# Optimization experiments

Hardware: AMD Instinct MI355X
Metric: run time of the kernel (lower is better)

The kernel has to match this reference:

```python
import jax, jax.numpy as jnp
import numpy as np

EPS = 1e-5

def conv2d(x, w, b, pad):
    y = jax.lax.conv_general_dilated(x, w, (1, 1), [(pad, pad), (pad, pad)],
                                     dimension_numbers=('NCHW', 'OIHW', 'NCHW'))
    return y + b[None, :, None, None]

def batchnorm(x, g, be):
    # training-mode BN: biased batch statistics over (N,H,W)
    m = x.mean(axis=(0, 2, 3), keepdims=True)
    v = x.var(axis=(0, 2, 3), keepdims=True)
    return (x - m) * jax.lax.rsqrt(v + EPS) * g[None, :, None, None] + be[None, :, None, None]

def _bilinear_gather(x_flat, ys, xs, H, W):
    # x_flat: [B,C,H*W]; ys,xs: [B,H,W] float sample coords; zero outside borders
    y0f = jnp.floor(ys); x0f = jnp.floor(xs)
    wy = (ys - y0f)[:, None]; wx = (xs - x0f)[:, None]   # [B,1,H,W]
    y0 = y0f.astype(jnp.int32); x0 = x0f.astype(jnp.int32)

    def corner(iy, ix):
        valid = ((iy >= 0) & (iy < H) & (ix >= 0) & (ix < W)).astype(x_flat.dtype)
        idx = jnp.clip(iy, 0, H - 1) * W + jnp.clip(ix, 0, W - 1)   # [B,H,W]
        v = jax.vmap(lambda xf, i: xf[:, i])(x_flat, idx)           # [B,C,H,W]
        return v * valid[:, None]

    v00 = corner(y0, x0);     v01 = corner(y0, x0 + 1)
    v10 = corner(y0 + 1, x0); v11 = corner(y0 + 1, x0 + 1)
    return v00 * (1 - wy) * (1 - wx) + v01 * (1 - wy) * wx + v10 * wy * (1 - wx) + v11 * wy * wx

def dcn(x, w, b, ow, ob):
    # modulated deformable conv (DCNv2), k=3, stride=1, pad=1
    B, C, H, W = x.shape
    K = 9
    om = conv2d(x, ow, ob, 1)                 # [B,27,H,W]
    dy = om[:, :K]; dx = om[:, K:2 * K]; m = jax.nn.sigmoid(om[:, 2 * K:])
    x_flat = x.reshape(B, C, H * W)
    base_y = jnp.arange(H, dtype=x.dtype)[None, :, None]
    base_x = jnp.arange(W, dtype=x.dtype)[None, None, :]
    out = jnp.zeros((B, w.shape[0], H, W), dtype=x.dtype)
    for k in range(K):  # fixed 9 kernel taps
        ky, kx = k // 3 - 1, k % 3 - 1
        ys = base_y + ky + dy[:, k]
        xs = base_x + kx + dx[:, k]
        samp = _bilinear_gather(x_flat, ys, xs, H, W)        # [B,C,H,W]
        out = out + jnp.einsum('bchw,oc->bohw', samp * m[:, k][:, None], w[:, :, k // 3, k % 3])
    return out + b[None, :, None, None]

def setup_inputs() -> dict:
    key = jax.random.key(0)
    ks = iter(jax.random.split(key, 64))
    B, H, W, C = 2, 256, 256, 64
    NB = 16
    f32 = jnp.float32
    d = {}
    for name in ['LowDEM', 'Point_Ele', 'Slope', 'Distance', 'Level']:
        d[name] = jax.random.normal(next(ks), (B, 1, H, W), dtype=f32)
    s = 0.05
    d['conv0_w'] = jax.random.normal(next(ks), (1, 3, 1, 1), f32) * s
    d['conv0_b'] = jnp.zeros((1,), f32)
    d['conv1_w'] = jax.random.normal(next(ks), (C, 1, 9, 9), f32) * s
    d['conv1_b'] = jnp.zeros((C,), f32)
    d['rb_w1'] = jax.random.normal(next(ks), (NB, C, C, 3, 3), f32) * s
    d['rb_b1'] = jnp.zeros((NB, C), f32)
    d['rb_g1'] = jnp.ones((NB, C), f32)
    d['rb_be1'] = jnp.zeros((NB, C), f32)
    d['rb_w2'] = jax.random.normal(next(ks), (NB, C, C, 3, 3), f32) * s
    d['rb_b2'] = jnp.zeros((NB, C), f32)
    d['rb_g2'] = jnp.ones((NB, C), f32)
    d['rb_be2'] = jnp.zeros((NB, C), f32)
    d['conv2_w'] = jax.random.normal(next(ks), (C, C, 3, 3), f32) * s
    d['conv2_b'] = jnp.zeros((C,), f32)
    d['bn2_g'] = jnp.ones((C,), f32)
    d['bn2_be'] = jnp.zeros((C,), f32)
    for nm, cout in [('dc2', C), ('dc3', C), ('dc4', 1)]:
        d[nm + '_w'] = jax.random.normal(next(ks), (cout, C, 3, 3), f32) * s
        d[nm + '_b'] = jnp.zeros((cout,), f32)
        d[nm + '_ow'] = jax.random.normal(next(ks), (27, C, 3, 3), f32) * 0.01
        d[nm + '_ob'] = jnp.zeros((27,), f32)
    d['conv4_w'] = jax.random.normal(next(ks), (1, 1, 1, 1), f32) * s
    d['conv4_b'] = jnp.zeros((1,), f32)
    return d

def reference(LowDEM, Point_Ele, Slope, Distance, Level,
              conv0_w, conv0_b, conv1_w, conv1_b,
              rb_w1, rb_b1, rb_g1, rb_be1, rb_w2, rb_b2, rb_g2, rb_be2,
              conv2_w, conv2_b, bn2_g, bn2_be,
              dc2_w, dc2_b, dc2_ow, dc2_ob,
              dc3_w, dc3_b, dc3_ow, dc3_ob,
              dc4_w, dc4_b, dc4_ow, dc4_ob,
              conv4_w, conv4_b):
    data = jnp.concatenate([Slope, Distance, Level], axis=1)
    error = conv2d(data, conv0_w, conv0_b, 0)
    lmask = (Level != 0).astype(LowDEM.dtype)
    error = error * lmask
    x = LowDEM * (1.0 - lmask) + Point_Ele + error
    x = conv2d(x, conv1_w, conv1_b, 4)
    y = x
    for i in range(rb_w1.shape[0]):  # fixed 16 residual blocks
        r = jax.nn.relu(batchnorm(conv2d(y, rb_w1[i], rb_b1[i], 1), rb_g1[i], rb_be1[i]))
        y = batchnorm(conv2d(r, rb_w2[i], rb_b2[i], 1), rb_g2[i], rb_be2[i]) + y
    x = batchnorm(conv2d(y, conv2_w, conv2_b, 1), bn2_g, bn2_be) + x
    x = jax.nn.relu(dcn(x, dc2_w, dc2_b, dc2_ow, dc2_ob))
    x = jax.nn.relu(dcn(x, dc3_w, dc3_b, dc3_ow, dc3_ob))
    x = dcn(x, dc4_w, dc4_b, dc4_ow, dc4_ob)
    return conv2d(x, conv4_w, conv4_b, 0)
```

## Files before the change

kernel.cpp:

```cpp
#include <hip/hip_runtime.h>
#include <cmath>

typedef unsigned short ushort_t;
typedef __attribute__((ext_vector_type(8))) short bf16x8;
typedef __attribute__((ext_vector_type(4))) float f32x4;

static constexpr int Bn   = 2;
static constexpr int Hn   = 256;
static constexpr int Wn   = 256;
static constexpr int HW   = Hn * Wn;
static constexpr int CHW  = 64 * HW;
static constexpr int NCHW = Bn * CHW;
static constexpr int NPIX = Bn * HW;
static constexpr float EPSv = 1e-5f;
static constexpr float INV_N = 1.0f / 131072.0f;
static constexpr int NSLOT = 64;
static constexpr int STSLOT = NSLOT * 128;
static constexpr int WFL = 73728;

__device__ inline uint32_t bf16_rne(float f) {
  uint32_t u = __float_as_uint(f);
  return (u + 0x7FFFu + ((u >> 16) & 1u)) >> 16;
}
__device__ inline void split_hl(float v, uint32_t& h, uint32_t& l) {
  h = bf16_rne(v);
  l = bf16_rne(v - __uint_as_float(h << 16)) & 0xFFFFu;
}
__device__ inline bf16x8 lds_ld16(const ushort_t* p) {
  union { bf16x8 v; uint2 u[2]; } r;
  r.u[0] = *(const uint2*)p;
  r.u[1] = *(const uint2*)(p + 4);
  return r.v;
}

typedef __attribute__((address_space(1))) const void glb_void;
typedef __attribute__((address_space(3))) void lds_void;
__device__ inline void gld_lds16(const void* g, void* l) {
  __builtin_amdgcn_global_load_lds((glb_void*)g, (lds_void*)l, 16, 0, 0);
}

__global__ void transpose_w_kernel(const float* __restrict__ in, float* __restrict__ out,
                                   int NB, int OC, int IC, int K) {
  int total = NB * OC * IC * K;
  for (int i = blockIdx.x * blockDim.x + threadIdx.x; i < total; i += gridDim.x * blockDim.x) {
    int k  = i % K;
    int t  = i / K;
    int ic = t % IC; t /= IC;
    int oc = t % OC;
    int nb = t / OC;
    out[(((size_t)nb * IC + ic) * K + k) * OC + oc] = in[i];
  }
}

__global__ void prep_wfrag(const float* __restrict__ w, ushort_t* __restrict__ out,
                           int NGp, int ocreal, int wlstride, int olstride) {
  int layer = blockIdx.y;
  int elems = 9 * 2 * NGp * 64 * 8;
  int idx = blockIdx.x * 256 + threadIdx.x;
  if (idx >= elems) return;
  int j = idx & 7, lane = (idx >> 3) & 63;
  int rest = idx >> 9;
  int g = rest % NGp; rest /= NGp;
  int ih = rest & 1, tap = rest >> 1;
  int oc = g * 16 + (lane & 15);
  int ic = ih * 32 + (lane >> 4) * 8 + j;
  float v = 0.0f;
  if (oc < ocreal) v = w[(size_t)layer * wlstride + (oc * 64 + ic) * 9 + tap];
  uint32_t hi, lo;
  split_hl(v, hi, lo);
  out[(size_t)layer * olstride + idx] = (ushort_t)hi;
  out[(size_t)layer * olstride + elems + idx] = (ushort_t)lo;
}

__global__ void prep_kernel(const float* __restrict__ LowDEM, const float* __restrict__ Point_Ele,
                            const float* __restrict__ Slope, const float* __restrict__ Distance,
                            const float* __restrict__ Level, const float* __restrict__ w0,
                            const float* __restrict__ b0, float* __restrict__ x0) {
  int i = blockIdx.x * blockDim.x + threadIdx.x;
  if (i >= NPIX) return;
  float lv  = Level[i];
  float err = w0[0] * Slope[i] + w0[1] * Distance[i] + w0[2] * lv + b0[0];
  float lm  = (lv != 0.0f) ? 1.0f : 0.0f;
  x0[i] = LowDEM[i] * (1.0f - lm) + Point_Ele[i] + err * lm;
}

__global__ __launch_bounds__(256, 2)
void conv9x9_kernel(const float* __restrict__ in, const float* __restrict__ wT,
                    const float* __restrict__ bias, float* __restrict__ out,
                    uint32_t* __restrict__ hiP, uint32_t* __restrict__ loP) {
  const int tx = threadIdx.x & 15, ty = threadIdx.x >> 4;
  const int w0 = blockIdx.x * 16, h0 = blockIdx.y * 16, b = blockIdx.z;
  __shared__ float lds[24 * 24];
  for (int idx = threadIdx.x; idx < 576; idx += 256) {
    int yy = idx / 24, xx = idx - yy * 24;
    int gy = h0 + yy - 4, gx = w0 + xx - 4;
    float v = 0.0f;
    if ((unsigned)gy < 256u && (unsigned)gx < 256u) v = in[b * HW + gy * 256 + gx];
    lds[idx] = v;
  }
  __syncthreads();
  float acc[64];
#pragma unroll
  for (int o = 0; o < 64; o++) acc[o] = 0.0f;
#pragma unroll 1
  for (int i = 0; i < 9; i++) {
#pragma unroll
    for (int j = 0; j < 9; j++) {
      float v = lds[(ty + i) * 24 + tx + j];
      const float* wp = wT + (i * 9 + j) * 64;
#pragma unroll
      for (int o = 0; o < 64; o++) acc[o] = fmaf(v, wp[o], acc[o]);
    }
  }
  const int p = (h0 + ty) * 256 + (w0 + tx);
  if (hiP) {
    float* op = out + ((size_t)b * HW + p) * 64;
#pragma unroll
    for (int o4 = 0; o4 < 16; o4++) {
      float4 v;
      v.x = acc[o4 * 4 + 0] + bias[o4 * 4 + 0];
      v.y = acc[o4 * 4 + 1] + bias[o4 * 4 + 1];
      v.z = acc[o4 * 4 + 2] + bias[o4 * 4 + 2];
      v.w = acc[o4 * 4 + 3] + bias[o4 * 4 + 3];
      *(float4*)(op + o4 * 4) = v;
    }
    uint32_t* hb = hiP + ((size_t)b * HW + p) * 32;
    uint32_t* lb = loP + ((size_t)b * HW + p) * 32;
#pragma unroll
    for (int o2 = 0; o2 < 32; o2++) {
      float v0 = acc[o2 * 2] + bias[o2 * 2];
      float v1 = acc[o2 * 2 + 1] + bias[o2 * 2 + 1];
      uint32_t h0v, l0v, h1v, l1v;
      split_hl(v0, h0v, l0v);
      split_hl(v1, h1v, l1v);
      hb[o2] = h0v | (h1v << 16);
      lb[o2] = l0v | (l1v << 16);
    }
  } else {
    float* op = out + (size_t)b * CHW + p;
#pragma unroll
    for (int o = 0; o < 64; o++) op[o * HW] = acc[o] + bias[o];
  }
}

template <int NG, int MODE, int STATS, int OCLIM, int HASBIAS, int WRITEY, int INHWC>
__global__ __launch_bounds__(256, 3)
void mfma_conv3(const float* __restrict__ in, const float* __restrict__ skip,
                const ushort_t* __restrict__ wf,
                const float* __restrict__ bias, const float* __restrict__ stats_in,
                const float* __restrict__ gg, const float* __restrict__ be,
                float* __restrict__ stats_out, float* __restrict__ yout,
                float* __restrict__ out) {
  const int tid  = threadIdx.x;
  const int lane = tid & 63, wid = tid >> 6;
  const int m = lane & 15, quad = lane >> 4;
  const int x0 = blockIdx.x * 16, y0 = blockIdx.y * 4, b = blockIdx.z;
  constexpr int WT = 2 * NG * 64 * 8;
  __shared__ __align__(16) ushort_t xh[108 * 68];
  __shared__ __align__(16) ushort_t xl[108 * 68];
  __shared__ float s_sc[MODE ? 64 : 1], s_sh[MODE ? 64 : 1];
  __shared__ float red[STATS ? 2 * 4 * 64 : 1];
  if (MODE) {
    if (tid < 64) {
      float sum = 0.0f, sq = 0.0f;
      for (int sl = 0; sl < NSLOT; sl++) {
        sum += stats_in[sl * 128 + tid];
        sq  += stats_in[sl * 128 + 64 + tid];
      }
      float mn = sum * INV_N, var = sq * INV_N - mn * mn;
      float s = gg[tid] * rsqrtf(var + EPSv);
      s_sc[tid] = s;
      s_sh[tid] = be[tid] - mn * s;
    }
    __syncthreads();
  }
  const float* inb = in + (size_t)b * CHW;
  const float* skb = MODE == 2 ? skip + (size_t)b * CHW : nullptr;
  float* ytb = WRITEY ? yout + (size_t)b * CHW : nullptr;
  uint32_t* xh32 = (uint32_t*)xh;
  uint32_t* xl32 = (uint32_t*)xl;
#pragma unroll
  for (int t = 0; t < 14; t++) {
    int idx = t * 256 + tid;
    if (idx < 3456) {
      int r, icp;
      if (INHWC) { icp = idx & 31; r = idx >> 5; }
      else       { r = idx % 108; icp = idx / 108; }
      int row = r / 18, col = r - row * 18;
      int gy = y0 - 1 + row, gx = x0 - 1 + col;
      float v0 = 0.0f, v1 = 0.0f;
      if ((unsigned)gy < 256u && (unsigned)gx < 256u) {
        int ic = icp * 2;
        if (INHWC) {
          float2 vv = *(const float2*)&inb[(size_t)(gy * 256 + gx) * 64 + ic];
          v0 = vv.x; v1 = vv.y;
        } else {
          v0 = inb[ic * HW + gy * 256 + gx];
          v1 = inb[(ic + 1) * HW + gy * 256 + gx];
        }
        if (MODE == 1) {
          v0 = fmaxf(fmaf(v0, s_sc[ic], s_sh[ic]), 0.0f);
          v1 = fmaxf(fmaf(v1, s_sc[ic + 1], s_sh[ic + 1]), 0.0f);
        }
        if (MODE == 2) {
          v0 = fmaf(v0, s_sc[ic], s_sh[ic]) + skb[ic * HW + gy * 256 + gx];
          v1 = fmaf(v1, s_sc[ic + 1], s_sh[ic + 1]) + skb[(ic + 1) * HW + gy * 256 + gx];
          if (WRITEY && row >= 1 && row <= 4 && col >= 1 && col <= 16) {
            ytb[ic * HW + gy * 256 + gx] = v0;
            ytb[(ic + 1) * HW + gy * 256 + gx] = v1;
          }
        }
      }
      uint32_t h0, l0, h1, l1;
      split_hl(v0, h0, l0);
      split_hl(v1, h1, l1);
      xh32[r * 34 + icp] = h0 | (h1 << 16);
      xl32[r * 34 + icp] = l0 | (l1 << 16);
    }
  }
  __syncthreads();
  f32x4 acc[NG];
#pragma unroll
  for (int g = 0; g < NG; g++) acc[g] = (f32x4){0.0f, 0.0f, 0.0f, 0.0f};

  const bf16x8* wfh = (const bf16x8*)wf;
  const bf16x8* wfl = (const bf16x8*)(wf + 9 * WT);

#pragma unroll 1
  for (int tap = 0; tap < 9; tap++) {
    bf16x8 bh[2][NG], bl[2][NG];
#pragma unroll
    for (int ih = 0; ih < 2; ih++)
#pragma unroll
      for (int g = 0; g < NG; g++) {
        int fi = ((tap * 2 + ih) * NG + g) * 64 + lane;
        bh[ih][g] = wfh[fi];
        bl[ih][g] = wfl[fi];
      }
    const int dy = tap / 3 - 1, dx = tap % 3 - 1;
    const int spat = (wid + dy + 1) * 18 + (m + dx + 1);
#pragma unroll
    for (int ih = 0; ih < 2; ih++) {
      const int base = spat * 68 + ih * 32 + quad * 8;
      bf16x8 ah = lds_ld16(xh + base);
      bf16x8 al = lds_ld16(xl + base);
#pragma unroll
      for (int g = 0; g < NG; g++) {
        acc[g] = __builtin_amdgcn_mfma_f32_16x16x32_bf16(ah, bh[ih][g], acc[g], 0, 0, 0);
        acc[g] = __builtin_amdgcn_mfma_f32_16x16x32_bf16(al, bh[ih][g], acc[g], 0, 0, 0);
        acc[g] = __builtin_amdgcn_mfma_f32_16x16x32_bf16(ah, bl[ih][g], acc[g], 0, 0, 0);
      }
    }
  }
  const int py = y0 + wid;
  float* ob = out + (size_t)b * OCLIM * HW + py * 256 + x0 + quad * 4;
#pragma unroll
  for (int g = 0; g < NG; g++) {
    int oc = g * 16 + m;
    if (oc < OCLIM) {
      float bv = HASBIAS ? bias[oc] : 0.0f;
#pragma unroll
      for (int r = 0; r < 4; r++) ob[oc * HW + r] = acc[g][r] + bv;
    }
    if (STATS) {
      float s  = acc[g][0] + acc[g][1] + acc[g][2] + acc[g][3];
      float s2 = acc[g][0] * acc[g][0] + acc[g][1] * acc[g][1] +
                 acc[g][2] * acc[g][2] + acc[g][3] * acc[g][3];
      s  += __shfl_xor(s, 16, 64);  s  += __shfl_xor(s, 32, 64);
      s2 += __shfl_xor(s2, 16, 64); s2 += __shfl_xor(s2, 32, 64);
      if (lane < 16) {
        red[(0 * 4 + wid) * 64 + g * 16 + lane] = s;
        red[(1 * 4 + wid) * 64 + g * 16 + lane] = s2;
      }
    }
  }
  if (STATS) {
    __syncthreads();
    if (tid < 128) {
      int oc = tid & 63, which = tid >> 6;
      float tot = red[(which * 4 + 0) * 64 + oc] + red[(which * 4 + 1) * 64 + oc] +
                  red[(which * 4 + 2) * 64 + oc] + red[(which * 4 + 3) * 64 + oc];
      int slot = (blockIdx.y * 16 + blockIdx.x) & (NSLOT - 1);
      atomicAdd(&stats_out[slot * 128 + which * 64 + oc], tot);
    }
  }
}

__global__ __launch_bounds__(256, 3)
void mfma_conv3_dma(const ushort_t* __restrict__ hiP, const ushort_t* __restrict__ loP,
                    const ushort_t* __restrict__ wf, const float* __restrict__ zeroPg,
                    float* __restrict__ stats_out, float* __restrict__ out) {
  const int tid  = threadIdx.x;
  const int lane = tid & 63, wid = tid >> 6;
  const int m = lane & 15, quad = lane >> 4;
  const int x0 = blockIdx.x * 16, y0 = blockIdx.y * 8, b = blockIdx.z;
  __shared__ __align__(16) ushort_t xs[2880 * 8];
  __shared__ float red[2 * 4 * 64];
  const size_t bimg = (size_t)b * HW;
  for (int g = wid; g < 45; g += 4) {
    int q  = g * 64 + lane;
    int pl = q >= 1440;
    int r  = q - (pl ? 1440 : 0);
    int s  = r >> 3, jl = r & 7;
    int js = jl ^ (s & 7);
    int row = s / 18, col = s - row * 18;
    int gy = y0 - 1 + row, gx = x0 - 1 + col;
    const ushort_t* src = (const ushort_t*)zeroPg;
    if ((unsigned)gy < 256u && (unsigned)gx < 256u)
      src = (pl ? loP : hiP) + ((bimg + (size_t)(gy * 256 + gx)) << 6) + (js << 3);
    gld_lds16(src, (void*)&xs[(size_t)g * 512]);
  }
  __syncthreads();

  f32x4 acc[2][4];
#pragma unroll
  for (int t = 0; t < 2; t++)
#pragma unroll
    for (int g = 0; g < 4; g++) acc[t][g] = (f32x4){0.0f, 0.0f, 0.0f, 0.0f};
  const bf16x8* wfh = (const bf16x8*)wf;
  const bf16x8* wfl8 = (const bf16x8*)(wf + 9 * 4096);

#pragma unroll 1
  for (int tap = 0; tap < 9; tap++) {
    bf16x8 bh[2][4], bl[2][4];
#pragma unroll
    for (int ih = 0; ih < 2; ih++)
#pragma unroll
      for (int g = 0; g < 4; g++) {
        int fi = ((tap * 2 + ih) * 4 + g) * 64 + lane;
        bh[ih][g] = wfh[fi];
        bl[ih][g] = wfl8[fi];
      }
    const int dy = tap / 3 - 1, dxx = tap % 3 - 1;
    const int scol = m + dxx + 1;
#pragma unroll
    for (int t = 0; t < 2; t++) {
      const int s  = (wid * 2 + t + dy + 1) * 18 + scol;
      const int s7 = s & 7;
#pragma unroll
      for (int ih = 0; ih < 2; ih++) {
        const int ch = s * 8 + ((ih * 4 + quad) ^ s7);
        bf16x8 ah = *(const bf16x8*)&xs[ch * 8];
        bf16x8 al = *(const bf16x8*)&xs[ch * 8 + 11520];
#pragma unroll
        for (int g = 0; g < 4; g++) {
          acc[t][g] = __builtin_amdgcn_mfma_f32_16x16x32_bf16(ah, bh[ih][g], acc[t][g], 0, 0, 0);
          acc[t][g] = __builtin_amdgcn_mfma_f32_16x16x32_bf16(al, bh[ih][g], acc[t][g], 0, 0, 0);
          acc[t][g] = __builtin_amdgcn_mfma_f32_16x16x32_bf16(ah, bl[ih][g], acc[t][g], 0, 0, 0);
        }
      }
    }
  }
#pragma unroll
  for (int g = 0; g < 4; g++) {
    int oc = g * 16 + m;
    float s = 0.0f, s2 = 0.0f;
#pragma unroll
    for (int t = 0; t < 2; t++) {
      const int py = y0 + wid * 2 + t;
      float* ob = out + ((size_t)b * HW + (size_t)py * 256 + x0) * 64;
#pragma unroll
      for (int r = 0; r < 4; r++) {
        float v = acc[t][g][r];
        ob[(quad * 4 + r) * 64 + oc] = v;
        s += v;
        s2 += v * v;
      }
    }
    s  += __shfl_xor(s, 16, 64);  s  += __shfl_xor(s, 32, 64);
    s2 += __shfl_xor(s2, 16, 64); s2 += __shfl_xor(s2, 32, 64);
    if (lane < 16) {
      red[(0 * 4 + wid) * 64 + g * 16 + lane] = s;
      red[(1 * 4 + wid) * 64 + g * 16 + lane] = s2;
    }
  }
  __syncthreads();
  if (tid < 128) {
    int oc = tid & 63, which = tid >> 6;
    float tot = red[(which * 4 + 0) * 64 + oc] + red[(which * 4 + 1) * 64 + oc] +
                red[(which * 4 + 2) * 64 + oc] + red[(which * 4 + 3) * 64 + oc];
    int slot = (blockIdx.y * 16 + blockIdx.x) & (NSLOT - 1);
    atomicAdd(&stats_out[slot * 128 + which * 64 + oc], tot);
  }
}

__global__ __launch_bounds__(256, 3)
void ofs_conv_dma(const ushort_t* __restrict__ hiP, const ushort_t* __restrict__ loP,
                  const ushort_t* __restrict__ wf, const float* __restrict__ zeroPg,
                  const float* __restrict__ bias, float* __restrict__ out) {
  const int tid  = threadIdx.x;
  const int lane = tid & 63, wid = tid >> 6;
  const int m = lane & 15, quad = lane >> 4;
  const int x0 = blockIdx.x * 16, y0 = blockIdx.y * 8, b = blockIdx.z;
  __shared__ __align__(16) ushort_t xs[2880 * 8];
  const size_t bimg = (size_t)b * HW;
  for (int g = wid; g < 45; g += 4) {
    int q  = g * 64 + lane;
    int pl = q >= 1440;
    int r  = q - (pl ? 1440 : 0);
    int s  = r >> 3, jl = r & 7;
    int js = jl ^ (s & 7);
    int row = s / 18, col = s - row * 18;
    int gy = y0 - 1 + row, gx = x0 - 1 + col;
    const ushort_t* src = (const ushort_t*)zeroPg;
    if ((unsigned)gy < 256u && (unsigned)gx < 256u)
      src = (pl ? loP : hiP) + ((bimg + (size_t)(gy * 256 + gx)) << 6) + (js << 3);
    gld_lds16(src, (void*)&xs[(size_t)g * 512]);
  }
  __syncthreads();

  f32x4 acc[2][2];
#pragma unroll
  for (int t = 0; t < 2; t++)
#pragma unroll
    for (int g = 0; g < 2; g++) acc[t][g] = (f32x4){0.0f, 0.0f, 0.0f, 0.0f};
  const bf16x8* wfh = (const bf16x8*)wf;
  const bf16x8* wfl8 = (const bf16x8*)(wf + 9 * 2048);

#pragma unroll 1
  for (int tap = 0; tap < 9; tap++) {
    bf16x8 bh[2][2], bl[2][2];
#pragma unroll
    for (int ih = 0; ih < 2; ih++)
#pragma unroll
      for (int g = 0; g < 2; g++) {
        int fi = ((tap * 2 + ih) * 2 + g) * 64 + lane;
        bh[ih][g] = wfh[fi];
        bl[ih][g] = wfl8[fi];
      }
    const int dy = tap / 3 - 1, dxx = tap % 3 - 1;
    const int scol = m + dxx + 1;
#pragma unroll
    for (int t = 0; t < 2; t++) {
      const int s  = (wid * 2 + t + dy + 1) * 18 + scol;
      const int s7 = s & 7;
#pragma unroll
      for (int ih = 0; ih < 2; ih++) {
        const int ch = s * 8 + ((ih * 4 + quad) ^ s7);
        bf16x8 ah = *(const bf16x8*)&xs[ch * 8];
        bf16x8 al = *(const bf16x8*)&xs[ch * 8 + 11520];
#pragma unroll
        for (int g = 0; g < 2; g++) {
          acc[t][g] = __builtin_amdgcn_mfma_f32_16x16x32_bf16(ah, bh[ih][g], acc[t][g], 0, 0, 0);
          acc[t][g] = __builtin_amdgcn_mfma_f32_16x16x32_bf16(al, bh[ih][g], acc[t][g], 0, 0, 0);
          acc[t][g] = __builtin_amdgcn_mfma_f32_16x16x32_bf16(ah, bl[ih][g], acc[t][g], 0, 0, 0);
        }
      }
    }
  }
#pragma unroll
  for (int g = 0; g < 2; g++) {
    int oc = g * 16 + m;
    if (oc < 27) {
      float bv = bias[oc];
#pragma unroll
      for (int t = 0; t < 2; t++) {
        const int py = y0 + wid * 2 + t;
        float* ob = out + (size_t)b * 27 * HW + (size_t)oc * HW + py * 256 + x0 + quad * 4;
#pragma unroll
        for (int r = 0; r < 4; r++) ob[r] = acc[t][g][r] + bv;
      }
    }
  }
}

template <int TMODE>
__global__ __launch_bounds__(256, 8)
void bn_split_hwc(const float* __restrict__ t, const float* __restrict__ stats,
                  const float* __restrict__ g, const float* __restrict__ be,
                  const float* __restrict__ skip, float* __restrict__ yout,
                  uint32_t* __restrict__ hiP, uint32_t* __restrict__ loP) {
  __shared__ float part[2][4][64];
  __shared__ float s_sc[64], s_sh[64];
  const int tid = threadIdx.x;
  {
    int c = tid & 63, q = tid >> 6;
    float sum = 0.0f, sq = 0.0f;
    for (int sl = q * 16; sl < q * 16 + 16; sl++) {
      sum += stats[sl * 128 + c];
      sq  += stats[sl * 128 + 64 + c];
    }
    part[0][q][c] = sum;
    part[1][q][c] = sq;
  }
  __syncthreads();
  if (tid < 64) {
    int c = tid;
    float sum = part[0][0][c] + part[0][1][c] + part[0][2][c] + part[0][3][c];
    float sq  = part[1][0][c] + part[1][1][c] + part[1][2][c] + part[1][3][c];
    float mn  = sum * INV_N;
    float var = sq * INV_N - mn * mn;
    float s   = g[c] * rsqrtf(var + EPSv);
    s_sc[c] = s;
    s_sh[c] = be[c] - mn * s;
  }
  __syncthreads();
  const int blk = blockIdx.x;
  const int b  = blk >> 10;
  const int p0 = (blk & 1023) * 64;
  const size_t base = ((size_t)b * HW + p0) * 64;
  uint32_t* hb = hiP + ((size_t)b * HW + p0) * 32;
  uint32_t* lb = loP + ((size_t)b * HW + p0) * 32;
#pragma unroll
  for (int i = 0; i < 8; i++) {
    int idx = i * 256 + tid;
    int p = idx >> 5, c2 = idx & 31;
    size_t off = base + (size_t)p * 64 + c2 * 2;
    float2 v = *(const float2*)&t[off];
    float v0 = fmaf(v.x, s_sc[c2 * 2],     s_sh[c2 * 2]);
    float v1 = fmaf(v.y, s_sc[c2 * 2 + 1], s_sh[c2 * 2 + 1]);
    if (TMODE == 1) {
      v0 = fmaxf(v0, 0.0f);
      v1 = fmaxf(v1, 0.0f);
    } else {
      float2 k = *(const float2*)&skip[off];
      v0 += k.x; v1 += k.y;
      float2 y2; y2.x = v0; y2.y = v1;
      *(float2*)&yout[off] = y2;
    }
    uint32_t h0v, l0v, h1v, l1v;
    split_hl(v0, h0v, l0v);
    split_hl(v1, h1v, l1v);
    hb[p * 32 + c2] = h0v | (h1v << 16);
    lb[p * 32 + c2] = l0v | (l1v << 16);
  }
}

__global__ __launch_bounds__(256, 8)
void bn_add_hwc(const float* __restrict__ t, const float* __restrict__ stats,
                const float* __restrict__ g, const float* __restrict__ be,
                const float* __restrict__ skip, float* __restrict__ xout,
                uint32_t* __restrict__ hiP, uint32_t* __restrict__ loP) {
  __shared__ float part[2][4][64];
  __shared__ float s_sc[64], s_sh[64];
  const int tid = threadIdx.x;
  {
    int c = tid & 63, q = tid >> 6;
    float sum = 0.0f, sq = 0.0f;
    for (int sl = q * 16; sl < q * 16 + 16; sl++) {
      sum += stats[sl * 128 + c];
      sq  += stats[sl * 128 + 64 + c];
    }
    part[0][q][c] = sum;
    part[1][q][c] = sq;
  }
  __syncthreads();
  if (tid < 64) {
    int c = tid;
    float sum = part[0][0][c] + part[0][1][c] + part[0][2][c] + part[0][3][c];
    float sq  = part[1][0][c] + part[1][1][c] + part[1][2][c] + part[1][3][c];
    float mn  = sum * INV_N;
    float var = sq * INV_N - mn * mn;
    float s   = g[c] * rsqrtf(var + EPSv);
    s_sc[c] = s;
    s_sh[c] = be[c] - mn * s;
  }
  __syncthreads();
  const int blk = blockIdx.x;
  const int b  = blk >> 10;
  const int p0 = (blk & 1023) * 64;
  const size_t base4 = (((size_t)b * HW + p0) * 64) >> 2;
  const float4* t4 = (const float4*)t;
  const float4* k4 = (const float4*)skip;
  float4* x4 = (float4*)xout;
  uint32_t* hb = hiP + ((size_t)b * HW + p0) * 32;
  uint32_t* lb = loP + ((size_t)b * HW + p0) * 32;
#pragma unroll
  for (int i = 0; i < 4; i++) {
    int idx = i * 256 + tid;
    int c = (idx & 15) * 4;
    int p = idx >> 4;
    float4 v = t4[base4 + idx], k = k4[base4 + idx], r;
    r.x = fmaf(v.x, s_sc[c],     s_sh[c])     + k.x;
    r.y = fmaf(v.y, s_sc[c + 1], s_sh[c + 1]) + k.y;
    r.z = fmaf(v.z, s_sc[c + 2], s_sh[c + 2]) + k.z;
    r.w = fmaf(v.w, s_sc[c + 3], s_sh[c + 3]) + k.w;
    x4[base4 + idx] = r;
    uint32_t h0v, l0v, h1v, l1v, h2v, l2v, h3v, l3v;
    split_hl(r.x, h0v, l0v); split_hl(r.y, h1v, l1v);
    split_hl(r.z, h2v, l2v); split_hl(r.w, h3v, l3v);
    uint2 hv = make_uint2(h0v | (h1v << 16), h2v | (h3v << 16));
    uint2 lv = make_uint2(l0v | (l1v << 16), l2v | (l3v << 16));
    *(uint2*)&hb[p * 32 + (c >> 1)] = hv;
    *(uint2*)&lb[p * 32 + (c >> 1)] = lv;
  }
}

__global__ void bn_apply_add_kernel(const float* __restrict__ t, const float* __restrict__ stats,
                                    const float* __restrict__ g, const float* __restrict__ be,
                                    const float* __restrict__ skip, float* __restrict__ out) {
  __shared__ float s_sc[64], s_sh[64];
  if (threadIdx.x < 64) {
    int c = threadIdx.x;
    float sum = 0.0f, sq = 0.0f;
    for (int sl = 0; sl < NSLOT; sl++) {
      sum += stats[sl * 128 + c];
      sq  += stats[sl * 128 + 64 + c];
    }
    float m   = sum * INV_N;
    float var = sq * INV_N - m * m;
    float s   = g[c] * rsqrtf(var + EPSv);
    s_sc[c] = s;
    s_sh[c] = be[c] - m * s;
  }
  __syncthreads();
  const float4* t4 = (const float4*)t;
  const float4* k4 = (const float4*)skip;
  float4* o4 = (float4*)out;
  const int n4 = NCHW / 4;
  for (int i = blockIdx.x * blockDim.x + threadIdx.x; i < n4; i += gridDim.x * blockDim.x) {
    int c = (i >> 14) & 63;
    float s = s_sc[c], h = s_sh[c];
    float4 v = t4[i], kk = k4[i], r;
    r.x = fmaf(v.x, s, h) + kk.x;
    r.y = fmaf(v.y, s, h) + kk.y;
    r.z = fmaf(v.z, s, h) + kk.z;
    r.w = fmaf(v.w, s, h) + kk.w;
    o4[i] = r;
  }
}

__global__ __launch_bounds__(256, 4)
void bn_tx_kernel(const float* __restrict__ t, const float* __restrict__ stats,
                  const float* __restrict__ g, const float* __restrict__ be,
                  const float* __restrict__ skip, float* __restrict__ outP,
                  float* __restrict__ outHWC) {
  __shared__ float tile[64][65];
  __shared__ float s_sc[64], s_sh[64];
  if (threadIdx.x < 64) {
    int c = threadIdx.x;
    float sum = 0.0f, sq = 0.0f;
    for (int sl = 0; sl < NSLOT; sl++) {
      sum += stats[sl * 128 + c];
      sq  += stats[sl * 128 + 64 + c];
    }
    float m   = sum * INV_N;
    float var = sq * INV_N - m * m;
    float s   = g[c] * rsqrtf(var + EPSv);
    s_sc[c] = s;
    s_sh[c] = be[c] - m * s;
  }
  __syncthreads();
  const int blk = blockIdx.x;
  const int b = blk >> 10;
  const int p0 = (blk & 1023) * 64;
  const float* tb = t + (size_t)b * CHW;
  const float* kb = skip + (size_t)b * CHW;
  float* oP = outP + (size_t)b * CHW;
  float* oH = outHWC + (size_t)b * CHW;
#pragma unroll
  for (int i = 0; i < 16; i++) {
    int idx = i * 256 + threadIdx.x;
    int c = idx >> 6, p = idx & 63;
    float v = fmaf(tb[c * HW + p0 + p], s_sc[c], s_sh[c]) + kb[c * HW + p0 + p];
    oP[c * HW + p0 + p] = v;
    tile[c][p] = v;
  }
  __syncthreads();
#pragma unroll
  for (int i = 0; i < 16; i++) {
    int idx = i * 256 + threadIdx.x;
    int p = idx >> 6, c = idx & 63;
    oH[(size_t)(p0 + p) * 64 + c] = tile[c][p];
  }
}

template <int NG, int FINAL>
__global__ __launch_bounds__(256, 4)
void dcn_mfma(const float* __restrict__ xhwc, const float* __restrict__ om,
              const ushort_t* __restrict__ wf, const float* __restrict__ bias,
              const float* __restrict__ c4w, const float* __restrict__ c4b,
              float* __restrict__ out) {
  const int tid  = threadIdx.x;
  const int lane = tid & 63, wid = tid >> 6;
  const int m = lane & 15, quad = lane >> 4;
  const int x0 = blockIdx.x * 16, y0 = blockIdx.y * 4, b = blockIdx.z;
  constexpr int WT = 2 * NG * 64 * 8;
  __shared__ __align__(16) ushort_t sh[2][64 * 64];
  __shared__ __align__(16) ushort_t sl[2][64 * 64];
  const int gp = tid >> 2, c4 = tid & 3;
  const int gpy = y0 + (gp >> 4), gxx = x0 + (gp & 15);
  const int psw = gp & 3;
  const float* xb  = xhwc + (size_t)b * CHW;
  const float* omb = om + (size_t)b * 27 * HW + gpy * 256 + gxx;

  auto gather = [&](int tap, int buf) {
    float dyv = omb[tap * HW];
    float dxv = omb[(9 + tap) * HW];
    float mo  = omb[(18 + tap) * HW];
    float mk  = 1.0f / (1.0f + __expf(-mo));
    float ys = fminf(fmaxf((float)(gpy + tap / 3 - 1) + dyv, -2.0f), 258.0f);
    float xs = fminf(fmaxf((float)(gxx + tap % 3 - 1) + dxv, -2.0f), 258.0f);
    float y0f = floorf(ys), x0f = floorf(xs);
    float wy = ys - y0f, wx = xs - x0f;
    int yi = (int)y0f, xi = (int)x0f;
    float vy0 = ((unsigned)yi       < 256u) ? 1.0f : 0.0f;
    float vy1 = ((unsigned)(yi + 1) < 256u) ? 1.0f : 0.0f;
    float vx0 = ((unsigned)xi       < 256u) ? 1.0f : 0.0f;
    float vx1 = ((unsigned)(xi + 1) < 256u) ? 1.0f : 0.0f;
    int cy0 = min(max(yi, 0), 255), cy1 = min(max(yi + 1, 0), 255);
    int cx0 = min(max(xi, 0), 255), cx1 = min(max(xi + 1, 0), 255);
    float W00 = (1.0f - wy) * (1.0f - wx) * mk * vy0 * vx0;
    float W01 = (1.0f - wy) * wx * mk * vy0 * vx1;
    float W10 = wy * (1.0f - wx) * mk * vy1 * vx0;
    float W11 = wy * wx * mk * vy1 * vx1;
    const float* p00 = xb + (size_t)(cy0 * 256 + cx0) * 64;
    const float* p01 = xb + (size_t)(cy0 * 256 + cx1) * 64;
    const float* p10 = xb + (size_t)(cy1 * 256 + cx0) * 64;
    const float* p11 = xb + (size_t)(cy1 * 256 + cx1) * 64;
#pragma unroll
    for (int j = 0; j < 4; j++) {
      const int k = c4 + 4 * j;
      float4 a  = *(const float4*)(p00 + k * 4);
      float4 b2 = *(const float4*)(p01 + k * 4);
      float4 c2 = *(const float4*)(p10 + k * 4);
      float4 d2 = *(const float4*)(p11 + k * 4);
      float s0 = W00 * a.x + W01 * b2.x + W10 * c2.x + W11 * d2.x;
      float s1 = W00 * a.y + W01 * b2.y + W10 * c2.y + W11 * d2.y;
      float s2 = W00 * a.z + W01 * b2.z + W10 * c2.z + W11 * d2.z;
      float s3 = W00 * a.w + W01 * b2.w + W10 * c2.w + W11 * d2.w;
      uint32_t h0, l0, h1, l1, h2, l2, h3, l3;
      split_hl(s0, h0, l0); split_hl(s1, h1, l1);
      split_hl(s2, h2, l2); split_hl(s3, h3, l3);
      int wi = gp * 64 + ((j ^ psw) * 16) + c4 * 4;
      *(uint2*)&sh[buf][wi] = make_uint2(h0 | (h1 << 16), h2 | (h3 << 16));
      *(uint2*)&sl[buf][wi] = make_uint2(l0 | (l1 << 16), l2 | (l3 << 16));
    }
  };

  f32x4 acc[NG];
#pragma unroll
  for (int g = 0; g < NG; g++) acc[g] = (f32x4){0.0f, 0.0f, 0.0f, 0.0f};
  const bf16x8* wfh = (const bf16x8*)wf;
  const bf16x8* wfl = (const bf16x8*)(wf + 9 * WT);
  const int px = wid * 16 + m;

  gather(0, 0);
  __syncthreads();
#pragma unroll 1
  for (int tap = 0; tap < 9; tap++) {
    const int cur = tap & 1;
    if (tap < 8) gather(tap + 1, cur ^ 1);
#pragma unroll
    for (int ih = 0; ih < 2; ih++) {
      const int c = ih * 2 + (quad >> 1), h = quad & 1;
      const int ri = px * 64 + ((c ^ (px & 3)) * 16) + h * 8;
      bf16x8 ah = *(const bf16x8*)&sh[cur][ri];
      bf16x8 al = *(const bf16x8*)&sl[cur][ri];
#pragma unroll
      for (int g = 0; g < NG; g++) {
        int fi = ((tap * 2 + ih) * NG + g) * 64 + lane;
        bf16x8 bh = wfh[fi], bl = wfl[fi];
        acc[g] = __builtin_amdgcn_mfma_f32_16x16x32_bf16(ah, bh, acc[g], 0, 0, 0);
        acc[g] = __builtin_amdgcn_mfma_f32_16x16x32_bf16(al, bh, acc[g], 0, 0, 0);
        acc[g] = __builtin_amdgcn_mfma_f32_16x16x32_bf16(ah, bl, acc[g], 0, 0, 0);
      }
    }
    __syncthreads();
  }
  const int py = y0 + wid;
  if (FINAL) {
    if (m == 0) {
      float* op = out + (size_t)b * HW + py * 256 + x0 + quad * 4;
#pragma unroll
      for (int r = 0; r < 4; r++) op[r] = c4w[0] * (acc[0][r] + bias[0]) + c4b[0];
    }
  } else {
    float* ob = out + (size_t)b * CHW + ((size_t)py * 256 + x0 + quad * 4) * 64 + m;
#pragma unroll
    for (int g = 0; g < NG; g++)
#pragma unroll
      for (int r = 0; r < 4; r++)
        ob[r * 64 + g * 16] = fmaxf(acc[g][r] + bias[g * 16 + m], 0.0f);
  }
}

extern "C" void kernel_launch(void* const* d_in, const int* in_sizes, int n_in,
                              void* d_out, int out_size, void* d_ws, size_t ws_size,
                              hipStream_t stream) {
  const float* LowDEM    = (const float*)d_in[0];
  const float* Point_Ele = (const float*)d_in[1];
  const float* Slope     = (const float*)d_in[2];
  const float* Distance  = (const float*)d_in[3];
  const float* Level     = (const float*)d_in[4];
  const float* conv0_w   = (const float*)d_in[5];
  const float* conv0_b   = (const float*)d_in[6];
  const float* conv1_w   = (const float*)d_in[7];
  const float* conv1_b   = (const float*)d_in[8];
  const float* rb_w1     = (const float*)d_in[9];
  const float* rb_g1     = (const float*)d_in[11];
  const float* rb_be1    = (const float*)d_in[12];
  const float* rb_w2     = (const float*)d_in[13];
  const float* rb_g2     = (const float*)d_in[15];
  const float* rb_be2    = (const float*)d_in[16];
  const float* conv2_w   = (const float*)d_in[17];
  const float* bn2_g     = (const float*)d_in[19];
  const float* bn2_be    = (const float*)d_in[20];
  const float* dc2_w     = (const float*)d_in[21];
  const float* dc2_b     = (const float*)d_in[22];
  const float* dc2_ow    = (const float*)d_in[23];
  const float* dc2_ob    = (const float*)d_in[24];
  const float* dc3_w     = (const float*)d_in[25];
  const float* dc3_b     = (const float*)d_in[26];
  const float* dc3_ow    = (const float*)d_in[27];
  const float* dc3_ob    = (const float*)d_in[28];
  const float* dc4_w     = (const float*)d_in[29];
  const float* dc4_b     = (const float*)d_in[30];
  const float* dc4_ow    = (const float*)d_in[31];
  const float* dc4_ob    = (const float*)d_in[32];
  const float* conv4_w   = (const float*)d_in[33];
  const float* conv4_b   = (const float*)d_in[34];

  float* x0   = (float*)d_ws;
  float* T1   = x0 + NPIX;
  ushort_t* WF = (ushort_t*)(T1 + 5184);
  float* stats = (float*)(WF + 39 * WFL);
  float* zpg   = stats + 33 * STSLOT;
  float* big   = zpg + 32;
  size_t used_small = (size_t)((char*)big - (char*)d_ws);
  bool fused = ws_size >= used_small + 5ull * NCHW * sizeof(float);

  float* bufX = big;
  float* bufT = bufX + NCHW;
  float* R3   = bufT + NCHW;
  float* R4   = R3 + NCHW;
  ushort_t* hiP = (ushort_t*)(R4 + NCHW);
  ushort_t* loP = hiP + NCHW;

  hipMemsetAsync(stats, 0, 33 * STSLOT * sizeof(float), stream);
  hipMemsetAsync(zpg, 0, 128, stream);

  transpose_w_kernel<<<32, 256, 0, stream>>>(conv1_w, T1, 1, 64, 1, 81);

  prep_wfrag<<<dim3(144, 16), 256, 0, stream>>>(rb_w1,   WF,            4, 64, 36864, WFL);
  prep_wfrag<<<dim3(144, 16), 256, 0, stream>>>(rb_w2,   WF + 16 * WFL, 4, 64, 36864, WFL);
  prep_wfrag<<<dim3(144, 1),  256, 0, stream>>>(conv2_w, WF + 32 * WFL, 4, 64, 36864, WFL);
  prep_wfrag<<<dim3(72, 1),   256, 0, stream>>>(dc2_ow,  WF + 33 * WFL, 2, 27, 15552, WFL);
  prep_wfrag<<<dim3(72, 1),   256, 0, stream>>>(dc3_ow,  WF + 34 * WFL, 2, 27, 15552, WFL);
  prep_wfrag<<<dim3(72, 1),   256, 0, stream>>>(dc4_ow,  WF + 35 * WFL, 2, 27, 15552, WFL);
  prep_wfrag<<<dim3(144, 1),  256, 0, stream>>>(dc2_w,   WF + 36 * WFL, 4, 64, 36864, WFL);
  prep_wfrag<<<dim3(144, 1),  256, 0, stream>>>(dc3_w,   WF + 37 * WFL, 4, 64, 36864, WFL);
  prep_wfrag<<<dim3(36, 1),   256, 0, stream>>>(dc4_w,   WF + 38 * WFL, 1, 1, 576, WFL);

  prep_kernel<<<(NPIX + 255) / 256, 256, 0, stream>>>(LowDEM, Point_Ele, Slope, Distance,
                                                      Level, conv0_w, conv0_b, x0);

  dim3 grid16(16, 16, 2);
  dim3 gmf(16, 64, 2);
  dim3 gmf8(16, 32, 2);

  conv9x9_kernel<<<grid16, 256, 0, stream>>>(x0, T1, conv1_b, bufX,
                                             fused ? (uint32_t*)hiP : nullptr,
                                             fused ? (uint32_t*)loP : nullptr);

  if (fused) {
    float* yA = R3;
    float* yB = R4;
    for (int i = 0; i < 16; i++) {
      mfma_conv3_dma<<<gmf8, 256, 0, stream>>>(hiP, loP, WF + (size_t)i * WFL, zpg,
                                               stats + (size_t)(2 * i) * STSLOT, bufT);
      bn_split_hwc<1><<<2048, 256, 0, stream>>>(
          bufT, stats + (size_t)(2 * i) * STSLOT, rb_g1 + i * 64, rb_be1 + i * 64,
          nullptr, nullptr, (uint32_t*)hiP, (uint32_t*)loP);
      mfma_conv3_dma<<<gmf8, 256, 0, stream>>>(hiP, loP, WF + (size_t)(16 + i) * WFL, zpg,
                                               stats + (size_t)(2 * i + 1) * STSLOT, bufT);
      const float* skp = (i == 0) ? bufX : ((i & 1) ? yA : yB);
      float* yo = (i & 1) ? yB : yA;
      bn_split_hwc<2><<<2048, 256, 0, stream>>>(
          bufT, stats + (size_t)(2 * i + 1) * STSLOT, rb_g2 + i * 64, rb_be2 + i * 64,
          skp, yo, (uint32_t*)hiP, (uint32_t*)loP);
    }
    mfma_conv3_dma<<<gmf8, 256, 0, stream>>>(hiP, loP, WF + (size_t)32 * WFL, zpg,
                                             stats + (size_t)32 * STSLOT, bufT);

    float* xT    = R4;
    float* d2out = R3;
    float* d3out = (float*)hiP;
    bn_add_hwc<<<2048, 256, 0, stream>>>(bufT, stats + 32 * STSLOT, bn2_g, bn2_be,
                                         bufX, xT, (uint32_t*)hiP, (uint32_t*)loP);
    ofs_conv_dma<<<gmf8, 256, 0, stream>>>(hiP, loP, WF + (size_t)33 * WFL, zpg,
                                           dc2_ob, bufT);
    dcn_mfma<4, 0><<<gmf, 256, 0, stream>>>(xT, bufT, WF + (size_t)36 * WFL, dc2_b,
                                            nullptr, nullptr, d2out);
    mfma_conv3<2, 0, 0, 27, 1, 0, 1><<<gmf, 256, 0, stream>>>(
        d2out, nullptr, WF + (size_t)34 * WFL, dc3_ob, nullptr, nullptr, nullptr,
        nullptr, nullptr, bufT);
    dcn_mfma<4, 0><<<gmf, 256, 0, stream>>>(d2out, bufT, WF + (size_t)37 * WFL, dc3_b,
                                            nullptr, nullptr, d3out);
    mfma_conv3<2, 0, 0, 27, 1, 0, 1><<<gmf, 256, 0, stream>>>(
        d3out, nullptr, WF + (size_t)35 * WFL, dc4_ob, nullptr, nullptr, nullptr,
        nullptr, nullptr, bufT);
    dcn_mfma<1, 1><<<gmf, 256, 0, stream>>>(d3out, bufT, WF + (size_t)38 * WFL, dc4_b,
                                            conv4_w, conv4_b, (float*)d_out);
  } else {
    float* bufT2 = R3;
    float* bufY  = R4;
    for (int i = 0; i < 16; i++) {
      const float* src = (i == 0) ? bufX : bufY;
      mfma_conv3<4, 0, 1, 64, 0, 0, 0><<<gmf, 256, 0, stream>>>(
          src, nullptr, WF + (size_t)i * WFL, nullptr, nullptr, nullptr, nullptr,
          stats + (2 * i) * STSLOT, nullptr, bufT);
      mfma_conv3<4, 1, 1, 64, 0, 0, 0><<<gmf, 256, 0, stream>>>(
          bufT, nullptr, WF + (size_t)(16 + i) * WFL, nullptr, stats + (2 * i) * STSLOT,
          rb_g1 + i * 64, rb_be1 + i * 64, stats + (2 * i + 1) * STSLOT, nullptr, bufT2);
      bn_apply_add_kernel<<<2048, 256, 0, stream>>>(bufT2, stats + (2 * i + 1) * STSLOT,
                                                    rb_g2 + i * 64, rb_be2 + i * 64, src, bufY);
    }
    mfma_conv3<4, 0, 1, 64, 0, 0, 0><<<gmf, 256, 0, stream>>>(
        bufY, nullptr, WF + (size_t)32 * WFL, nullptr, nullptr, nullptr, nullptr,
        stats + 32 * STSLOT, nullptr, bufT);
    float* xT    = R4;
    float* d2out = R3;
    float* d3out = R4;
    bn_tx_kernel<<<2048, 256, 0, stream>>>(bufT, stats + 32 * STSLOT, bn2_g, bn2_be,
                                           bufX, bufX, xT);
    mfma_conv3<2, 0, 0, 27, 1, 0, 0><<<gmf, 256, 0, stream>>>(
        bufX, nullptr, WF + (size_t)33 * WFL, dc2_ob, nullptr, nullptr, nullptr,
        nullptr, nullptr, bufT);
    dcn_mfma<4, 0><<<gmf, 256, 0, stream>>>(xT, bufT, WF + (size_t)36 * WFL, dc2_b,
                                            nullptr, nullptr, d2out);
    mfma_conv3<2, 0, 0, 27, 1, 0, 1><<<gmf, 256, 0, stream>>>(
        d2out, nullptr, WF + (size_t)34 * WFL, dc3_ob, nullptr, nullptr, nullptr,
        nullptr, nullptr, bufT);
    dcn_mfma<4, 0><<<gmf, 256, 0, stream>>>(d2out, bufT, WF + (size_t)37 * WFL, dc3_b,
                                            nullptr, nullptr, d3out);
    mfma_conv3<2, 0, 0, 27, 1, 0, 1><<<gmf, 256, 0, stream>>>(
        d3out, nullptr, WF + (size_t)35 * WFL, dc4_ob, nullptr, nullptr, nullptr,
        nullptr, nullptr, bufT);
    dcn_mfma<1, 1><<<gmf, 256, 0, stream>>>(d3out, bufT, WF + (size_t)38 * WFL, dc4_b,
                                            conv4_w, conv4_b, (float*)d_out);
  }
}
```

Before: 2.317 ms.

## Split conv3 MFMA work by output-channel group per wave instead of rows

Each wave in the 3x3 MFMA conv now owns one 16-channel output group across all 8 rows, instead of 2 rows across all 64 channels. Each wave loads a quarter of the weight fragments per tap, which cuts register pressure and global weight traffic. In exchange each wave does four times as many LDS activation reads. Because each wave owns its channels, the BN statistics go straight to atomics, removing the shared-memory reduction and one barrier.

```diff
diff --git a/kernel.cpp b/kernel.cpp
--- a/kernel.cpp
+++ b/kernel.cpp
@@ -295,7 +295,6 @@
   const int m = lane & 15, quad = lane >> 4;
   const int x0 = blockIdx.x * 16, y0 = blockIdx.y * 8, b = blockIdx.z;
   __shared__ __align__(16) ushort_t xs[2880 * 8];
-  __shared__ float red[2 * 4 * 64];
   const size_t bimg = (size_t)b * HW;
   for (int g = wid; g < 45; g += 4) {
     int q  = g * 64 + lane;
@@ -312,75 +311,58 @@
   }
   __syncthreads();
 
-  f32x4 acc[2][4];
-#pragma unroll
-  for (int t = 0; t < 2; t++)
-#pragma unroll
-    for (int g = 0; g < 4; g++) acc[t][g] = (f32x4){0.0f, 0.0f, 0.0f, 0.0f};
+  f32x4 acc[8];
+#pragma unroll
+  for (int t = 0; t < 8; t++) acc[t] = (f32x4){0.0f, 0.0f, 0.0f, 0.0f};
   const bf16x8* wfh = (const bf16x8*)wf;
   const bf16x8* wfl8 = (const bf16x8*)(wf + 9 * 4096);
 
 #pragma unroll 1
   for (int tap = 0; tap < 9; tap++) {
-    bf16x8 bh[2][4], bl[2][4];
-#pragma unroll
-    for (int ih = 0; ih < 2; ih++)
-#pragma unroll
-      for (int g = 0; g < 4; g++) {
-        int fi = ((tap * 2 + ih) * 4 + g) * 64 + lane;
-        bh[ih][g] = wfh[fi];
-        bl[ih][g] = wfl8[fi];
-      }
+    bf16x8 bh[2], bl[2];
+#pragma unroll
+    for (int ih = 0; ih < 2; ih++) {
+      int fi = ((tap * 2 + ih) * 4 + wid) * 64 + lane;
+      bh[ih] = wfh[fi];
+      bl[ih] = wfl8[fi];
+    }
     const int dy = tap / 3 - 1, dxx = tap % 3 - 1;
     const int scol = m + dxx + 1;
 #pragma unroll
-    for (int t = 0; t < 2; t++) {
-      const int s  = (wid * 2 + t + dy + 1) * 18 + scol;
+    for (int t = 0; t < 8; t++) {
+      const int s  = (t + dy + 1) * 18 + scol;
       const int s7 = s & 7;
 #pragma unroll
       for (int ih = 0; ih < 2; ih++) {
         const int ch = s * 8 + ((ih * 4 + quad) ^ s7);
         bf16x8 ah = *(const bf16x8*)&xs[ch * 8];
         bf16x8 al = *(const bf16x8*)&xs[ch * 8 + 11520];
-#pragma unroll
-        for (int g = 0; g < 4; g++) {
-          acc[t][g] = __builtin_amdgcn_mfma_f32_16x16x32_bf16(ah, bh[ih][g], acc[t][g], 0, 0, 0);
-          acc[t][g] = __builtin_amdgcn_mfma_f32_16x16x32_bf16(al, bh[ih][g], acc[t][g], 0, 0, 0);
-          acc[t][g] = __builtin_amdgcn_mfma_f32_16x16x32_bf16(ah, bl[ih][g], acc[t][g], 0, 0, 0);
-        }
+        acc[t] = __builtin_amdgcn_mfma_f32_16x16x32_bf16(ah, bh[ih], acc[t], 0, 0, 0);
+        acc[t] = __builtin_amdgcn_mfma_f32_16x16x32_bf16(al, bh[ih], acc[t], 0, 0, 0);
+        acc[t] = __builtin_amdgcn_mfma_f32_16x16x32_bf16(ah, bl[ih], acc[t], 0, 0, 0);
       }
     }
   }
-#pragma unroll
-  for (int g = 0; g < 4; g++) {
-    int oc = g * 16 + m;
-    float s = 0.0f, s2 = 0.0f;
-#pragma unroll
-    for (int t = 0; t < 2; t++) {
-      const int py = y0 + wid * 2 + t;
-      float* ob = out + ((size_t)b * HW + (size_t)py * 256 + x0) * 64;
-#pragma unroll
-      for (int r = 0; r < 4; r++) {
-        float v = acc[t][g][r];
-        ob[(quad * 4 + r) * 64 + oc] = v;
-        s += v;
-        s2 += v * v;
-      }
-    }
-    s  += __shfl_xor(s, 16, 64);  s  += __shfl_xor(s, 32, 64);
-    s2 += __shfl_xor(s2, 16, 64); s2 += __shfl_xor(s2, 32, 64);
-    if (lane < 16) {
-      red[(0 * 4 + wid) * 64 + g * 16 + lane] = s;
-      red[(1 * 4 + wid) * 64 + g * 16 + lane] = s2;
-    }
-  }
-  __syncthreads();
-  if (tid < 128) {
-    int oc = tid & 63, which = tid >> 6;
-    float tot = red[(which * 4 + 0) * 64 + oc] + red[(which * 4 + 1) * 64 + oc] +
-                red[(which * 4 + 2) * 64 + oc] + red[(which * 4 + 3) * 64 + oc];
+  const int oc = wid * 16 + m;
+  float s = 0.0f, s2 = 0.0f;
+#pragma unroll
+  for (int t = 0; t < 8; t++) {
+    const int py = y0 + t;
+    float* ob = out + ((size_t)b * HW + (size_t)py * 256 + x0) * 64;
+#pragma unroll
+    for (int r = 0; r < 4; r++) {
+      float v = acc[t][r];
+      ob[(quad * 4 + r) * 64 + oc] = v;
+      s += v;
+      s2 += v * v;
+    }
+  }
+  s  += __shfl_xor(s, 16, 64);  s  += __shfl_xor(s, 32, 64);
+  s2 += __shfl_xor(s2, 16, 64); s2 += __shfl_xor(s2, 32, 64);
+  if (lane < 16) {
     int slot = (blockIdx.y * 16 + blockIdx.x) & (NSLOT - 1);
-    atomicAdd(&stats_out[slot * 128 + which * 64 + oc], tot);
+    atomicAdd(&stats_out[slot * 128 + oc], s);
+    atomicAdd(&stats_out[slot * 128 + 64 + oc], s2);
   }
 }
 
```

New measurement: 2.185 ms. 1.06x faster.

## Emit bf16 hi/lo planes from DCN and reuse DMA offset conv; rewarp conv3

Applied to the files above, without the earlier changes.

The first two DCN kernels now also write the split bf16 hi/lo planes of their output. The dc3 and dc4 offset convolutions can then use the LDS-DMA ofs_conv_dma kernel instead of the generic fp32 mfma_conv3. Separately, mfma_conv3_dma changes its warp split to 4 rows x 2 channel groups per warp. That halves the weight registers per warp and replaces the shared-memory stats reduction with per-warp atomics. The cost is extra plane writes from the DCN kernels and more atomic traffic.

```diff
diff --git a/kernel.cpp b/kernel.cpp
--- a/kernel.cpp
+++ b/kernel.cpp
@@ -295,7 +295,6 @@
   const int m = lane & 15, quad = lane >> 4;
   const int x0 = blockIdx.x * 16, y0 = blockIdx.y * 8, b = blockIdx.z;
   __shared__ __align__(16) ushort_t xs[2880 * 8];
-  __shared__ float red[2 * 4 * 64];
   const size_t bimg = (size_t)b * HW;
   for (int g = wid; g < 45; g += 4) {
     int q  = g * 64 + lane;
@@ -312,30 +311,32 @@
   }
   __syncthreads();
 
-  f32x4 acc[2][4];
-#pragma unroll
-  for (int t = 0; t < 2; t++)
-#pragma unroll
-    for (int g = 0; g < 4; g++) acc[t][g] = (f32x4){0.0f, 0.0f, 0.0f, 0.0f};
+  const int gsel = wid >> 1;
+  const int rsel = (wid & 1) * 4;
+  f32x4 acc[4][2];
+#pragma unroll
+  for (int t = 0; t < 4; t++)
+#pragma unroll
+    for (int g = 0; g < 2; g++) acc[t][g] = (f32x4){0.0f, 0.0f, 0.0f, 0.0f};
   const bf16x8* wfh = (const bf16x8*)wf;
   const bf16x8* wfl8 = (const bf16x8*)(wf + 9 * 4096);
 
 #pragma unroll 1
   for (int tap = 0; tap < 9; tap++) {
-    bf16x8 bh[2][4], bl[2][4];
+    bf16x8 bh[2][2], bl[2][2];
 #pragma unroll
     for (int ih = 0; ih < 2; ih++)
 #pragma unroll
-      for (int g = 0; g < 4; g++) {
-        int fi = ((tap * 2 + ih) * 4 + g) * 64 + lane;
+      for (int g = 0; g < 2; g++) {
+        int fi = ((tap * 2 + ih) * 4 + gsel * 2 + g) * 64 + lane;
         bh[ih][g] = wfh[fi];
         bl[ih][g] = wfl8[fi];
       }
     const int dy = tap / 3 - 1, dxx = tap % 3 - 1;
     const int scol = m + dxx + 1;
 #pragma unroll
-    for (int t = 0; t < 2; t++) {
-      const int s  = (wid * 2 + t + dy + 1) * 18 + scol;
+    for (int t = 0; t < 4; t++) {
+      const int s  = (rsel + t + dy + 1) * 18 + scol;
       const int s7 = s & 7;
 #pragma unroll
       for (int ih = 0; ih < 2; ih++) {
@@ -343,7 +344,7 @@
         bf16x8 ah = *(const bf16x8*)&xs[ch * 8];
         bf16x8 al = *(const bf16x8*)&xs[ch * 8 + 11520];
 #pragma unroll
-        for (int g = 0; g < 4; g++) {
+        for (int g = 0; g < 2; g++) {
           acc[t][g] = __builtin_amdgcn_mfma_f32_16x16x32_bf16(ah, bh[ih][g], acc[t][g], 0, 0, 0);
           acc[t][g] = __builtin_amdgcn_mfma_f32_16x16x32_bf16(al, bh[ih][g], acc[t][g], 0, 0, 0);
           acc[t][g] = __builtin_amdgcn_mfma_f32_16x16x32_bf16(ah, bl[ih][g], acc[t][g], 0, 0, 0);
@@ -351,13 +352,14 @@
       }
     }
   }
-#pragma unroll
-  for (int g = 0; g < 4; g++) {
-    int oc = g * 16 + m;
+  const int slot = (blockIdx.y * 16 + blockIdx.x) & (NSLOT - 1);
+#pragma unroll
+  for (int g = 0; g < 2; g++) {
+    const int oc = gsel * 32 + g * 16 + m;
     float s = 0.0f, s2 = 0.0f;
 #pragma unroll
-    for (int t = 0; t < 2; t++) {
-      const int py = y0 + wid * 2 + t;
+    for (int t = 0; t < 4; t++) {
+      const int py = y0 + rsel + t;
       float* ob = out + ((size_t)b * HW + (size_t)py * 256 + x0) * 64;
 #pragma unroll
       for (int r = 0; r < 4; r++) {
@@ -370,17 +372,9 @@
     s  += __shfl_xor(s, 16, 64);  s  += __shfl_xor(s, 32, 64);
     s2 += __shfl_xor(s2, 16, 64); s2 += __shfl_xor(s2, 32, 64);
     if (lane < 16) {
-      red[(0 * 4 + wid) * 64 + g * 16 + lane] = s;
-      red[(1 * 4 + wid) * 64 + g * 16 + lane] = s2;
-    }
-  }
-  __syncthreads();
-  if (tid < 128) {
-    int oc = tid & 63, which = tid >> 6;
-    float tot = red[(which * 4 + 0) * 64 + oc] + red[(which * 4 + 1) * 64 + oc] +
-                red[(which * 4 + 2) * 64 + oc] + red[(which * 4 + 3) * 64 + oc];
-    int slot = (blockIdx.y * 16 + blockIdx.x) & (NSLOT - 1);
-    atomicAdd(&stats_out[slot * 128 + which * 64 + oc], tot);
+      atomicAdd(&stats_out[slot * 128 + oc], s);
+      atomicAdd(&stats_out[slot * 128 + 64 + oc], s2);
+    }
   }
 }
 
@@ -665,12 +659,13 @@
   }
 }
 
-template <int NG, int FINAL>
+template <int NG, int FINAL, int PLANES>
 __global__ __launch_bounds__(256, 4)
 void dcn_mfma(const float* __restrict__ xhwc, const float* __restrict__ om,
               const ushort_t* __restrict__ wf, const float* __restrict__ bias,
               const float* __restrict__ c4w, const float* __restrict__ c4b,
-              float* __restrict__ out) {
+              float* __restrict__ out,
+              ushort_t* __restrict__ hiO, ushort_t* __restrict__ loO) {
   const int tid  = threadIdx.x;
   const int lane = tid & 63, wid = tid >> 6;
   const int m = lane & 15, quad = lane >> 4;
@@ -766,12 +761,21 @@
       for (int r = 0; r < 4; r++) op[r] = c4w[0] * (acc[0][r] + bias[0]) + c4b[0];
     }
   } else {
-    float* ob = out + (size_t)b * CHW + ((size_t)py * 256 + x0 + quad * 4) * 64 + m;
+    size_t pbase = ((size_t)b * HW + (size_t)py * 256 + x0 + quad * 4) * 64 + m;
+    float* ob = out + pbase;
 #pragma unroll
     for (int g = 0; g < NG; g++)
 #pragma unroll
-      for (int r = 0; r < 4; r++)
-        ob[r * 64 + g * 16] = fmaxf(acc[g][r] + bias[g * 16 + m], 0.0f);
+      for (int r = 0; r < 4; r++) {
+        float v = fmaxf(acc[g][r] + bias[g * 16 + m], 0.0f);
+        ob[r * 64 + g * 16] = v;
+        if (PLANES) {
+          uint32_t h, l;
+          split_hl(v, h, l);
+          hiO[pbase + r * 64 + g * 16] = (ushort_t)h;
+          loO[pbase + r * 64 + g * 16] = (ushort_t)l;
+        }
+      }
   }
 }
 
@@ -875,23 +879,22 @@
 
     float* xT    = R4;
     float* d2out = R3;
-    float* d3out = (float*)hiP;
+    float* d3out = bufX;
     bn_add_hwc<<<2048, 256, 0, stream>>>(bufT, stats + 32 * STSLOT, bn2_g, bn2_be,
                                          bufX, xT, (uint32_t*)hiP, (uint32_t*)loP);
     ofs_conv_dma<<<gmf8, 256, 0, stream>>>(hiP, loP, WF + (size_t)33 * WFL, zpg,
                                            dc2_ob, bufT);
-    dcn_mfma<4, 0><<<gmf, 256, 0, stream>>>(xT, bufT, WF + (size_t)36 * WFL, dc2_b,
-                                            nullptr, nullptr, d2out);
-    mfma_conv3<2, 0, 0, 27, 1, 0, 1><<<gmf, 256, 0, stream>>>(
-        d2out, nullptr, WF + (size_t)34 * WFL, dc3_ob, nullptr, nullptr, nullptr,
-        nullptr, nullptr, bufT);
-    dcn_mfma<4, 0><<<gmf, 256, 0, stream>>>(d2out, bufT, WF + (size_t)37 * WFL, dc3_b,
-                                            nullptr, nullptr, d3out);
-    mfma_conv3<2, 0, 0, 27, 1, 0, 1><<<gmf, 256, 0, stream>>>(
-        d3out, nullptr, WF + (size_t)35 * WFL, dc4_ob, nullptr, nullptr, nullptr,
-        nullptr, nullptr, bufT);
-    dcn_mfma<1, 1><<<gmf, 256, 0, stream>>>(d3out, bufT, WF + (size_t)38 * WFL, dc4_b,
-                                            conv4_w, conv4_b, (float*)d_out);
+    dcn_mfma<4, 0, 1><<<gmf, 256, 0, stream>>>(xT, bufT, WF + (size_t)36 * WFL, dc2_b,
+                                               nullptr, nullptr, d2out, hiP, loP);
+    ofs_conv_dma<<<gmf8, 256, 0, stream>>>(hiP, loP, WF + (size_t)34 * WFL, zpg,
+                                           dc3_ob, bufT);
+    dcn_mfma<4, 0, 1><<<gmf, 256, 0, stream>>>(d2out, bufT, WF + (size_t)37 * WFL, dc3_b,
+                                               nullptr, nullptr, d3out, hiP, loP);
+    ofs_conv_dma<<<gmf8, 256, 0, stream>>>(hiP, loP, WF + (size_t)35 * WFL, zpg,
+                                           dc4_ob, bufT);
+    dcn_mfma<1, 1, 0><<<gmf, 256, 0, stream>>>(d3out, bufT, WF + (size_t)38 * WFL, dc4_b,
+                                               conv4_w, conv4_b, (float*)d_out,
+                                               nullptr, nullptr);
   } else {
     float* bufT2 = R3;
     float* bufY  = R4;
@@ -917,17 +920,18 @@
     mfma_conv3<2, 0, 0, 27, 1, 0, 0><<<gmf, 256, 0, stream>>>(
         bufX, nullptr, WF + (size_t)33 * WFL, dc2_ob, nullptr, nullptr, nullptr,
         nullptr, nullptr, bufT);
-    dcn_mfma<4, 0><<<gmf, 256, 0, stream>>>(xT, bufT, WF + (size_t)36 * WFL, dc2_b,
-                                            nullptr, nullptr, d2out);
+    dcn_mfma<4, 0, 0><<<gmf, 256, 0, stream>>>(xT, bufT, WF + (size_t)36 * WFL, dc2_b,
+                                               nullptr, nullptr, d2out, nullptr, nullptr);
     mfma_conv3<2, 0, 0, 27, 1, 0, 1><<<gmf, 256, 0, stream>>>(
         d2out, nullptr, WF + (size_t)34 * WFL, dc3_ob, nullptr, nullptr, nullptr,
         nullptr, nullptr, bufT);
-    dcn_mfma<4, 0><<<gmf, 256, 0, stream>>>(d2out, bufT, WF + (size_t)37 * WFL, dc3_b,
-                                            nullptr, nullptr, d3out);
+    dcn_mfma<4, 0, 0><<<gmf, 256, 0, stream>>>(d2out, bufT, WF + (size_t)37 * WFL, dc3_b,
+                                               nullptr, nullptr, d3out, nullptr, nullptr);
     mfma_conv3<2, 0, 0, 27, 1, 0, 1><<<gmf, 256, 0, stream>>>(
         d3out, nullptr, WF + (size_t)35 * WFL, dc4_ob, nullptr, nullptr, nullptr,
         nullptr, nullptr, bufT);
-    dcn_mfma<1, 1><<<gmf, 256, 0, stream>>>(d3out, bufT, WF + (size_t)38 * WFL, dc4_b,
-                                            conv4_w, conv4_b, (float*)d_out);
-  }
-}
+    dcn_mfma<1, 1, 0><<<gmf, 256, 0, stream>>>(d3out, bufT, WF + (size_t)38 * WFL, dc4_b,
+                                               conv4_w, conv4_b, (float*)d_out,
+                                               nullptr, nullptr);
+  }
+}
```

Result: faster. 2.026 ms (-12.6%).
